# Kernel optimization log

Hardware: AMD Instinct MI355X
Metric: run time of the kernel (lower is better)

## Reference

```python
import jax, jax.numpy as jnp
import numpy as np

D_MODEL = 512
D_STATE = 16
D_INNER = 2 * D_MODEL  # expand_factor=2
IN_CH = 256
B_SZ, H_SZ, W_SZ = 4, 32, 32


def setup_inputs() -> dict:
    key = jax.random.key(0)
    ks = jax.random.split(key, 24)
    f = jax.random.normal
    inp = {}
    inp["x_V"] = f(ks[0], (B_SZ, IN_CH, H_SZ, W_SZ), jnp.float32)
    inp["x_I"] = f(ks[1], (B_SZ, IN_CH, H_SZ, W_SZ), jnp.float32)
    # channel_reduce: 1x1 conv + BN (inference stats)
    inp["conv_red_w"] = f(ks[2], (D_MODEL, IN_CH), jnp.float32) * 0.05
    inp["bn_red_g"] = jnp.ones((D_MODEL,), jnp.float32)
    inp["bn_red_b"] = jnp.zeros((D_MODEL,), jnp.float32)
    inp["bn_red_m"] = jnp.zeros((D_MODEL,), jnp.float32)
    inp["bn_red_v"] = jnp.ones((D_MODEL,), jnp.float32)
    # channel_restore: 1x1 conv + BN
    inp["conv_res_w"] = f(ks[3], (IN_CH, D_MODEL), jnp.float32) * 0.05
    inp["bn_res_g"] = jnp.ones((IN_CH,), jnp.float32)
    inp["bn_res_b"] = jnp.zeros((IN_CH,), jnp.float32)
    inp["bn_res_m"] = jnp.zeros((IN_CH,), jnp.float32)
    inp["bn_res_v"] = jnp.ones((IN_CH,), jnp.float32)
    # lambda_predictor convs (1x1 on pooled features == linear)
    inp["lam_w1"] = f(ks[4], (D_MODEL // 4, D_MODEL * 2), jnp.float32) * 0.05
    inp["lam_b1"] = jnp.zeros((D_MODEL // 4,), jnp.float32)
    inp["lam_w2"] = f(ks[5], (2, D_MODEL // 4), jnp.float32) * 0.05
    inp["lam_b2"] = jnp.zeros((2,), jnp.float32)
    # two SimplifiedMamba2Blocks
    for i, p in enumerate(["V", "I"]):
        kk = jax.random.split(ks[6 + i], 6)
        inp[p + "_in_w"] = f(kk[0], (2 * D_INNER, D_MODEL), jnp.float32) * 0.03
        inp[p + "_out_w"] = f(kk[1], (D_MODEL, D_INNER), jnp.float32) * 0.03
        # A = -exp(A_log) in (-1, -0.05): stable decay
        inp[p + "_A_log"] = jnp.log(jax.random.uniform(kk[2], (D_INNER, D_STATE), jnp.float32, 0.05, 0.95))
        inp[p + "_B"] = f(kk[3], (D_INNER, D_STATE), jnp.float32) * 0.05
        inp[p + "_C"] = jnp.full((D_INNER, D_STATE), 0.01, jnp.float32)
        inp[p + "_ln_g"] = jnp.ones((D_MODEL,), jnp.float32)
        inp[p + "_ln_b"] = jnp.zeros((D_MODEL,), jnp.float32)
    inp["gate"] = jnp.asarray(0.1, jnp.float32)
    return inp


def _bn(x, g, b, m, v):
    # x: (B,C,H,W); inference-mode batchnorm
    return (x - m[:, None, None]) / jnp.sqrt(v[:, None, None] + 1e-5) * g[:, None, None] + b[:, None, None]


def _conv1x1(x, w):
    return jnp.einsum('bchw,oc->bohw', x, w)


def _ssm_scan(x_ssm, A, Bm, Cm, reverse):
    # x_ssm: (B,L,I); A,Bm,Cm: (I,S)
    bsz = x_ssm.shape[0]
    h0 = jnp.zeros((bsz, A.shape[0], A.shape[1]), x_ssm.dtype)

    def step(h, xt):  # xt: (B,I)
        h = jnp.clip(h * A + xt[:, :, None] * Bm, -10.0, 10.0)
        return h, jnp.einsum('bis,is->bi', h, Cm)

    _, ys = jax.lax.scan(step, h0, jnp.swapaxes(x_ssm, 0, 1), reverse=reverse)
    return jnp.swapaxes(ys, 0, 1)  # (B,L,I), in original time order


def _mamba(x, ln_g, ln_b, in_w, out_w, A_log, Bm, Cm):
    # LayerNorm
    mu = jnp.mean(x, -1, keepdims=True)
    var = jnp.mean((x - mu) ** 2, -1, keepdims=True)
    xn = (x - mu) / jnp.sqrt(var + 1e-5) * ln_g + ln_b
    xp = xn @ in_w.T  # (B,L,2*I)
    x_ssm, gate = jnp.split(xp, 2, axis=-1)
    A = jnp.clip(-jnp.exp(A_log), -10.0, -0.01)
    yf = _ssm_scan(x_ssm, A, Bm, Cm, False)
    yb = _ssm_scan(x_ssm, A, Bm, Cm, True)
    out = 0.5 * (yf + yb) * jax.nn.silu(gate)
    return out @ out_w.T


def reference(x_V, x_I, conv_red_w, bn_red_g, bn_red_b, bn_red_m, bn_red_v,
              conv_res_w, bn_res_g, bn_res_b, bn_res_m, bn_res_v,
              lam_w1, lam_b1, lam_w2, lam_b2,
              V_in_w, V_out_w, V_A_log, V_B, V_C, V_ln_g, V_ln_b,
              I_in_w, I_out_w, I_A_log, I_B, I_C, I_ln_g, I_ln_b, gate):
    B, _, H, W = x_V.shape
    xVr = jax.nn.relu(_bn(_conv1x1(x_V, conv_red_w), bn_red_g, bn_red_b, bn_red_m, bn_red_v))
    xIr = jax.nn.relu(_bn(_conv1x1(x_I, conv_red_w), bn_red_g, bn_red_b, bn_red_m, bn_red_v))
    # same spatial size -> adaptive pooling and [:B] slicing are identities
    conc = jnp.concatenate([xVr, xIr], axis=1)  # (B, 2*d_model, H, W)

    def lam(c):
        p = jnp.mean(c, axis=(2, 3))  # global avg pool -> (B, 2*d_model)
        h1 = jax.nn.relu(p @ lam_w1.T + lam_b1)
        return jax.nn.softmax(h1 @ lam_w2.T + lam_b2, axis=-1)  # (B,2)

    lamV = lam(conc)
    lamI = lam(conc)

    seq_V = jnp.swapaxes(xVr.reshape(B, D_MODEL, H * W), 1, 2)  # (B,L,D)
    seq_I = jnp.swapaxes(xIr.reshape(B, D_MODEL, H * W), 1, 2)

    outV_std = _mamba(seq_V, V_ln_g, V_ln_b, V_in_w, V_out_w, V_A_log, V_B, V_C)
    outI_std = _mamba(seq_I, I_ln_g, I_ln_b, I_in_w, I_out_w, I_A_log, I_B, I_C)
    outV_cross = _mamba(seq_V, V_ln_g, V_ln_b, V_in_w, V_out_w, V_A_log, jax.lax.stop_gradient(I_B), V_C)
    outI_cross = _mamba(seq_I, I_ln_g, I_ln_b, I_in_w, I_out_w, I_A_log, jax.lax.stop_gradient(V_B), I_C)

    outV = lamV[:, 0][:, None, None] * outV_std + lamV[:, 1][:, None, None] * outV_cross
    outI = lamI[:, 0][:, None, None] * outI_std + lamI[:, 1][:, None, None] * outI_cross

    featV = jnp.swapaxes(outV, 1, 2).reshape(B, D_MODEL, H, W)
    featI = jnp.swapaxes(outI, 1, 2).reshape(B, D_MODEL, H, W)
    featV = _bn(_conv1x1(featV, conv_res_w), bn_res_g, bn_res_b, bn_res_m, bn_res_v)
    featI = _bn(_conv1x1(featI, conv_res_w), bn_res_g, bn_res_b, bn_res_m, bn_res_v)

    g = jax.nn.sigmoid(gate)
    return (x_V + g * featV, x_I + g * featI)
```

## Files before the change

kernel.cpp:

```cpp
#include <hip/hip_runtime.h>
#include <hip/hip_bf16.h>
#include <math.h>

#define L_SZ 1024
#define DM   512
#define DI   1024
#define NS   16
#define CH   256

typedef float4 f4;
typedef __attribute__((ext_vector_type(8))) short short8;
typedef __attribute__((ext_vector_type(8))) unsigned short u16x8;
typedef __attribute__((ext_vector_type(4))) float f32x4;

__device__ __forceinline__ float bf2f(ushort u) {
    union { unsigned int i; float f; } x; x.i = ((unsigned int)u) << 16; return x.f;
}
__device__ __forceinline__ ushort f2bf(float f) {
    union { float f; unsigned int i; } x; x.f = f;
    unsigned int r = x.i + 0x7FFFu + ((x.i >> 16) & 1u);
    return (ushort)(r >> 16);
}
__device__ __forceinline__ uint pkbf(float a, float b) {
    union { __hip_bfloat162 h; uint u; } c;
    c.h = __float22bfloat162_rn(make_float2(a, b));
    return c.u;
}

#define GLOAD16(gp, lp) \
  __builtin_amdgcn_global_load_lds((const __attribute__((address_space(1))) void*)(gp), \
                                   (__attribute__((address_space(3))) void*)(lp), 16, 0, 0)

__global__ __launch_bounds__(256) void k_prep(
    const float* __restrict__ s0, const float* __restrict__ s1,
    const float* __restrict__ s2, const float* __restrict__ s3,
    const float* __restrict__ s4, const float* __restrict__ s5,
    ushort* __restrict__ d0, ushort* __restrict__ d1,
    ushort* __restrict__ d2, ushort* __restrict__ d3,
    ushort* __restrict__ d4, ushort* __restrict__ d5,
    const float* __restrict__ xv, const float* __restrict__ xi,
    ushort* __restrict__ xtv, ushort* __restrict__ xti,
    float* __restrict__ p, unsigned int* __restrict__ cnt)
{
    __shared__ float tile[32][36];
    const int bid = blockIdx.x;
    const int t = threadIdx.x;
    if (bid < 2304) {
        const float* s; ushort* d; int rel;
        if      (bid < 128)  { s = s0; d = d0; rel = bid; }
        else if (bid < 256)  { s = s1; d = d1; rel = bid - 128; }
        else if (bid < 1280) { s = s2; d = d2; rel = bid - 256; }
        else                 { s = s3; d = d3; rel = bid - 1280; }
        const int i = rel * 256 + t;
        f4 v = ((const f4*)s)[i];
        ushort4 o;
        o.x = f2bf(v.x); o.y = f2bf(v.y); o.z = f2bf(v.z); o.w = f2bf(v.w);
        ((ushort4*)d)[i] = o;
        return;
    }
    if (bid < 3328) {
        const int rel = (bid < 2816) ? bid - 2304 : bid - 2816;
        const float* wo = (bid < 2816) ? s4 : s5;
        ushort* wt      = (bid < 2816) ? d4 : d5;
        const int kt = rel & 31, dt = rel >> 5;
        const int d0_ = dt * 32, k0 = kt * 32;
        {
            int cc = t >> 3, ll4 = (t & 7) << 2;
            f4 v = *(const f4*)(wo + (size_t)(d0_ + cc) * 1024 + k0 + ll4);
            tile[cc][ll4 + 0] = v.x; tile[cc][ll4 + 1] = v.y;
            tile[cc][ll4 + 2] = v.z; tile[cc][ll4 + 3] = v.w;
        }
        __syncthreads();
        {
            int ll = t >> 3, cc4 = (t & 7) << 2;
            ushort4 o;
            o.x = f2bf(tile[cc4 + 0][ll]); o.y = f2bf(tile[cc4 + 1][ll]);
            o.z = f2bf(tile[cc4 + 2][ll]); o.w = f2bf(tile[cc4 + 3][ll]);
            *(ushort4*)(wt + (size_t)(k0 + ll) * 512 + d0_ + cc4) = o;
        }
        return;
    }
    if (bid < 5376) {
        const int rel = bid - 3328;
        const int l0 = (rel & 31) * 32, c0 = ((rel >> 5) & 7) * 32;
        const int z = rel >> 8;
        const int b = z & 3, st = z >> 2;
        const float* x = st ? xi : xv;
        ushort* xt = st ? xti : xtv;
        {
            int cc = t >> 3, ll4 = (t & 7) << 2;
            f4 v = *(const f4*)(x + ((size_t)(b * CH + c0 + cc)) * L_SZ + l0 + ll4);
            tile[cc][ll4 + 0] = v.x; tile[cc][ll4 + 1] = v.y;
            tile[cc][ll4 + 2] = v.z; tile[cc][ll4 + 3] = v.w;
        }
        __syncthreads();
        {
            int ll = t >> 3, cc4 = (t & 7) << 2;
            ushort4 o;
            o.x = f2bf(tile[cc4 + 0][ll]); o.y = f2bf(tile[cc4 + 1][ll]);
            o.z = f2bf(tile[cc4 + 2][ll]); o.w = f2bf(tile[cc4 + 3][ll]);
            *(ushort4*)(xt + ((size_t)(b * L_SZ + l0 + ll)) * CH + c0 + cc4) = o;
        }
        return;
    }
    const f4 z4 = {0.f, 0.f, 0.f, 0.f};
    ((f4*)p)[t]       = z4;
    ((f4*)p)[t + 256] = z4;
    ((f4*)p)[t + 512] = z4;
    ((f4*)p)[t + 768] = z4;
    if (t == 0) *cnt = 0u;
}

template<int MODE, int BM, int BN, int OS>
__global__ __launch_bounds__(256) void k_gemm(
    const ushort* __restrict__ A0, const ushort* __restrict__ A1,
    const ushort* __restrict__ B0, const ushort* __restrict__ B1,
    int K,
    float* __restrict__ o0, float* __restrict__ o1,
    ushort* __restrict__ ob0, ushort* __restrict__ ob1,
    ushort* __restrict__ sb0, ushort* __restrict__ sb1,
    const float* __restrict__ pg, const float* __restrict__ pb,
    const float* __restrict__ pm, const float* __restrict__ pv,
    const float* __restrict__ x0, const float* __restrict__ x1,
    const float* __restrict__ gate, float* __restrict__ pp)
{
    constexpr int MT   = BM / 32;
    constexpr int NT   = BN / 32;
    constexpr int ASEG = BM / 16;
    constexpr int NSEG = (BM + BN) / 16;
    constexpr int SPW  = NSEG / 4;
    __shared__ __align__(16) ushort Sl[2][(BM + BN) * 32];
    const int t = threadIdx.x;
    const int wv = t >> 6, lane = t & 63;
    const int n0 = blockIdx.x * BN, m0 = blockIdx.y * BM;
    const int st = blockIdx.z;
    const ushort* Ap = st ? A1 : A0;
    const ushort* Bp = st ? B1 : B0;
    const int wm = wv >> 1, wn = wv & 1;
    const int lrow = lane & 15, q = lane >> 4;
    f32x4 acc[MT][NT];
    #pragma unroll
    for (int a_ = 0; a_ < MT; ++a_)
        #pragma unroll
        for (int b_ = 0; b_ < NT; ++b_)
            acc[a_][b_] = (f32x4){0.f, 0.f, 0.f, 0.f};
    const int srow = lane >> 2;
    const int skk  = (((lane & 3) ^ ((lane >> 3) & 3)) << 3);
    const int koff = ((q ^ ((lrow >> 1) & 3)) << 3);
    #pragma unroll
    for (int s2 = 0; s2 < SPW; ++s2) {
        const int seg = wv * SPW + s2;
        const int grow = (seg < ASEG) ? (m0 + seg * 16 + srow)
                                      : (n0 + (seg - ASEG) * 16 + srow);
        const ushort* src = (seg < ASEG) ? Ap : Bp;
        GLOAD16(src + (size_t)grow * K + skk, &Sl[0][seg * 512]);
    }
    int cur = 0;
    for (int k0 = 0; k0 < K; k0 += 32) {
        if (k0 + 32 < K) {
            #pragma unroll
            for (int s2 = 0; s2 < SPW; ++s2) {
                const int seg = wv * SPW + s2;
                const int grow = (seg < ASEG) ? (m0 + seg * 16 + srow)
                                              : (n0 + (seg - ASEG) * 16 + srow);
                const ushort* src = (seg < ASEG) ? Ap : Bp;
                GLOAD16(src + (size_t)grow * K + (k0 + 32) + skk, &Sl[cur ^ 1][seg * 512]);
            }
            if constexpr (SPW == 2)      asm volatile("s_waitcnt vmcnt(2)" ::: "memory");
            else if constexpr (SPW == 3) asm volatile("s_waitcnt vmcnt(3)" ::: "memory");
            else                         asm volatile("s_waitcnt vmcnt(4)" ::: "memory");
        } else {
            asm volatile("s_waitcnt vmcnt(0)" ::: "memory");
        }
        __builtin_amdgcn_s_barrier();
        short8 af[MT], bfr[NT];
        #pragma unroll
        for (int mt = 0; mt < MT; ++mt)
            af[mt] = *(const short8*)&Sl[cur][(wm * (MT * 16) + mt * 16 + lrow) * 32 + koff];
        #pragma unroll
        for (int nt = 0; nt < NT; ++nt)
            bfr[nt] = *(const short8*)&Sl[cur][(BM + wn * (NT * 16) + nt * 16 + lrow) * 32 + koff];
        #pragma unroll
        for (int mt = 0; mt < MT; ++mt)
            #pragma unroll
            for (int nt = 0; nt < NT; ++nt) {
                if constexpr (MODE == 1)
                    acc[mt][nt] = __builtin_amdgcn_mfma_f32_16x16x32_bf16(bfr[nt], af[mt], acc[mt][nt], 0, 0, 0);
                else
                    acc[mt][nt] = __builtin_amdgcn_mfma_f32_16x16x32_bf16(af[mt], bfr[nt], acc[mt][nt], 0, 0, 0);
            }
        asm volatile("s_waitcnt lgkmcnt(0)" ::: "memory");
        __builtin_amdgcn_sched_barrier(0);
        __builtin_amdgcn_s_barrier();
        cur ^= 1;
    }
    if (MODE == 0) {
        ushort* sq = st ? ob1 : ob0;
        const int b = m0 >> 10;
        #pragma unroll
        for (int nt = 0; nt < NT; ++nt) {
            const int gn = n0 + wn * (NT * 16) + nt * 16 + lrow;
            const float s  = pg[gn] * rsqrtf(pv[gn] + 1e-5f);
            const float sh = pb[gn] - pm[gn] * s;
            float psum = 0.f;
            #pragma unroll
            for (int mt = 0; mt < MT; ++mt) {
                const int gm = m0 + wm * (MT * 16) + mt * 16 + q * 4;
                float v[4];
                #pragma unroll
                for (int r = 0; r < 4; ++r) {
                    v[r] = fmaxf(fmaf(acc[mt][nt][r], s, sh), 0.f);
                    psum += v[r];
                }
                const uint u01 = pkbf(v[0], v[1]);
                const uint u23 = pkbf(v[2], v[3]);
                ushort* bp = sq + (size_t)gm * DM + gn;
                bp[0]      = (ushort)u01;
                bp[DM]     = (ushort)(u01 >> 16);
                bp[2 * DM] = (ushort)u23;
                bp[3 * DM] = (ushort)(u23 >> 16);
            }
            psum += __shfl_xor(psum, 16, 64);
            psum += __shfl_xor(psum, 32, 64);
            if (q == 0)
                atomicAdd(pp + (b * 1024 + st * 512 + gn), psum * (1.0f / 1024.0f));
        }
    } else if (MODE == 1) {
        const bool isx = (n0 < 1024);
        ushort* xp = st ? ob1 : ob0;
        ushort* sp = st ? sb1 : sb0;
        #pragma unroll
        for (int mt = 0; mt < MT; ++mt) {
            const int gm = m0 + wm * (MT * 16) + mt * 16 + lrow;
            #pragma unroll
            for (int nt = 0; nt < NT; ++nt) {
                const int gnb = n0 + wn * (NT * 16) + nt * 16 + q * 4;
                if (isx) {
                    const uint u01 = pkbf(acc[mt][nt][0], acc[mt][nt][1]);
                    const uint u23 = pkbf(acc[mt][nt][2], acc[mt][nt][3]);
                    *(uint2*)(xp + (size_t)gm * DI + gnb) = make_uint2(u01, u23);
                } else {
                    float sv[4];
                    #pragma unroll
                    for (int r = 0; r < 4; ++r) {
                        const float v = acc[mt][nt][r];
                        sv[r] = v / (1.f + __expf(-v));
                    }
                    const uint u01 = pkbf(sv[0], sv[1]);
                    const uint u23 = pkbf(sv[2], sv[3]);
                    *(uint2*)(sp + (size_t)gm * DI + gnb - 1024) = make_uint2(u01, u23);
                }
            }
        }
    } else if (MODE == 2) {
        ushort* fp_ = st ? ob1 : ob0;
        #pragma unroll
        for (int nt = 0; nt < NT; ++nt) {
            const int gn = n0 + wn * (NT * 16) + nt * 16 + lrow;
            #pragma unroll
            for (int mt = 0; mt < MT; ++mt) {
                const int gm = m0 + wm * (MT * 16) + mt * 16 + q * 4;
                const uint u01 = pkbf(acc[mt][nt][0], acc[mt][nt][1]);
                const uint u23 = pkbf(acc[mt][nt][2], acc[mt][nt][3]);
                ushort* bp = fp_ + (size_t)gm * OS + gn;
                bp[0]      = (ushort)u01;
                bp[OS]     = (ushort)(u01 >> 16);
                bp[2 * OS] = (ushort)u23;
                bp[3 * OS] = (ushort)(u23 >> 16);
            }
        }
    } else {
        const float* xin = st ? x1 : x0;
        float* op = st ? o1 : o0;
        const float g = 1.f / (1.f + __expf(-gate[0]));
        #pragma unroll
        for (int nt = 0; nt < NT; ++nt) {
            const int gn = n0 + wn * (NT * 16) + nt * 16 + lrow;
            const float s  = pg[gn] * rsqrtf(pv[gn] + 1e-5f);
            const float sh = pb[gn] - pm[gn] * s;
            #pragma unroll
            for (int mt = 0; mt < MT; ++mt) {
                const int gmb = m0 + wm * (MT * 16) + mt * 16 + q * 4;
                const int b = gmb >> 10, l = gmb & 1023;
                const size_t off = ((size_t)(b * CH + gn)) * L_SZ + l;
                f4 xi = *(const f4*)(xin + off);
                f4 o;
                o.x = xi.x + g * fmaf(acc[mt][nt][0], s, sh);
                o.y = xi.y + g * fmaf(acc[mt][nt][1], s, sh);
                o.z = xi.z + g * fmaf(acc[mt][nt][2], s, sh);
                o.w = xi.w + g * fmaf(acc[mt][nt][3], s, sh);
                *(f4*)(op + off) = o;
            }
        }
    }
}

__global__ __launch_bounds__(256) void k_lam(
    const float* __restrict__ p, const float* __restrict__ w1,
    const float* __restrict__ b1, const float* __restrict__ w2,
    const float* __restrict__ b2, float* __restrict__ h1,
    float* __restrict__ lam, unsigned int* __restrict__ cnt)
{
    __shared__ float lsm[8];
    __shared__ unsigned int tick;
    const int t = threadIdx.x, lane = t & 63, wv = t >> 6;
    const int idx = blockIdx.x * 4 + wv;
    const int b = idx >> 7, j = idx & 127;
    const float* pb = p + b * 1024;
    const float* wr = w1 + j * 1024;
    float s = 0.f;
    #pragma unroll
    for (int k = 0; k < 16; ++k)
        s = fmaf(pb[lane + k * 64], wr[lane + k * 64], s);
    #pragma unroll
    for (int off = 1; off < 64; off <<= 1) s += __shfl_xor(s, off, 64);
    if (lane == 0) h1[idx] = fmaxf(s + b1[j], 0.f);
    __threadfence();
    __syncthreads();
    if (t == 0) tick = atomicAdd(cnt, 1u);
    __syncthreads();
    if (tick != 127u) return;
    __threadfence();
    {
        const int g32 = t >> 5, l32 = t & 31;
        const int bb = g32 >> 1, kk = g32 & 1;
        const float* hb = h1 + bb * 128;
        const float* wr2 = w2 + kk * 128;
        float ss = 0.f;
        #pragma unroll
        for (int u = 0; u < 4; ++u)
            ss = fmaf(hb[l32 + u * 32], wr2[l32 + u * 32], ss);
        #pragma unroll
        for (int off = 1; off < 32; off <<= 1) ss += __shfl_xor(ss, off, 64);
        if (l32 == 0) lsm[g32] = ss + b2[kk];
    }
    __syncthreads();
    if (t < 4) {
        const float a0 = lsm[t * 2], a1 = lsm[t * 2 + 1];
        const float m  = fmaxf(a0, a1);
        const float e0 = __expf(a0 - m), e1 = __expf(a1 - m);
        const float inv = 1.f / (e0 + e1);
        lam[t * 2 + 0] = e0 * inv;
        lam[t * 2 + 1] = e1 * inv;
    }
}

__global__ __launch_bounds__(256) void k_ln(
    const ushort* __restrict__ seq0, const ushort* __restrict__ seq1,
    const float* __restrict__ g0, const float* __restrict__ b0,
    const float* __restrict__ g1, const float* __restrict__ b1,
    ushort* __restrict__ ln0, ushort* __restrict__ ln1)
{
    const int t = threadIdx.x, lane = t & 63, wv = t >> 6;
    const int row = blockIdx.x * 4 + wv, st = blockIdx.y;
    const ushort* seq = st ? seq1 : seq0;
    const float* gg  = st ? g1 : g0;
    const float* bb  = st ? b1 : b0;
    ushort* ln = st ? ln1 : ln0;
    const u16x8 v = *(const u16x8*)(seq + (size_t)row * DM + lane * 8);
    float f[8];
    float s = 0.f, ss = 0.f;
    #pragma unroll
    for (int i = 0; i < 8; ++i) {
        f[i] = bf2f(v[i]);
        s += f[i];
        ss = fmaf(f[i], f[i], ss);
    }
    #pragma unroll
    for (int off = 1; off < 64; off <<= 1) {
        s += __shfl_xor(s, off, 64); ss += __shfl_xor(ss, off, 64);
    }
    const float mu = s * (1.f / 512.f);
    const float rstd = rsqrtf(ss * (1.f / 512.f) - mu * mu + 1e-5f);
    const f4 gv0 = *(const f4*)(gg + lane * 8);
    const f4 gv1 = *(const f4*)(gg + lane * 8 + 4);
    const f4 bv0 = *(const f4*)(bb + lane * 8);
    const f4 bv1 = *(const f4*)(bb + lane * 8 + 4);
    const float gvv[8] = {gv0.x, gv0.y, gv0.z, gv0.w, gv1.x, gv1.y, gv1.z, gv1.w};
    const float bvv[8] = {bv0.x, bv0.y, bv0.z, bv0.w, bv1.x, bv1.y, bv1.z, bv1.w};
    u16x8 o;
    #pragma unroll
    for (int i = 0; i < 8; i += 2) {
        const uint u = pkbf(fmaf((f[i]     - mu) * rstd, gvv[i],     bvv[i]),
                            fmaf((f[i + 1] - mu) * rstd, gvv[i + 1], bvv[i + 1]));
        o[i]     = (ushort)u;
        o[i + 1] = (ushort)(u >> 16);
    }
    *(u16x8*)(ln + (size_t)row * DM + lane * 8) = o;
}

__global__ __launch_bounds__(128, 4) void k_scan(
    const ushort* __restrict__ xsV, const ushort* __restrict__ xsI,
    const ushort* __restrict__ sgV, const ushort* __restrict__ sgI,
    const float* __restrict__ VA, const float* __restrict__ VB,
    const float* __restrict__ VC, const float* __restrict__ IA,
    const float* __restrict__ IB, const float* __restrict__ IC,
    const float* __restrict__ lam,
    ushort* __restrict__ yV, ushort* __restrict__ yI)
{
    __shared__ __align__(16) ushort xf[3][16][64];
    __shared__ __align__(16) ushort xb[3][16][64];
    const int t = threadIdx.x;
    const int shalf = t & 1;
    const int il = t >> 1;
    const int b = blockIdx.y;
    const int st = blockIdx.z >> 4, j = blockIdx.z & 15;
    const int c0 = blockIdx.x * 64;
    const ushort* xrow  = (st ? xsI : xsV) + (size_t)b * L_SZ * DI + c0;
    const ushort* sgrow = (st ? sgI : sgV) + (size_t)b * L_SZ * DI + c0;
    ushort* yrow        = (st ? yI  : yV ) + (size_t)b * L_SZ * DI + c0;
    const float* Alog = st ? IA : VA;
    const float* Cm   = st ? IC : VC;
    const float* Bown = st ? IB : VB;
    const float* Both = st ? VB : IB;
    const float lam0 = lam[b * 2 + 0], lam1 = lam[b * 2 + 1];
    float a[8], w[8], gf[8], gb[8];
    const int base = (c0 + il) * NS + shalf * 8;
    #pragma unroll
    for (int s = 0; s < 8; ++s) {
        a[s] = fminf(fmaxf(-__expf(Alog[base + s]), -10.f), -0.01f);
        w[s] = 0.5f * Cm[base + s] * fmaf(lam0, Bown[base + s], lam1 * Both[base + s]);
        gf[s] = 0.f; gb[s] = 0.f;
    }
    const int row0 = j << 6;
    const int srow = t >> 3;
    const int scol = (t & 7) << 3;
    ushort stash[32];

#define STAGE(PH, BUF) do { \
    int rf_ = row0 - 64 + (PH) * 16 + srow; rf_ = max(0, min(1023, rf_)); \
    GLOAD16(xrow + (size_t)rf_ * DI + scol, &xf[BUF][srow][0]); \
    int rb_ = row0 + 127 - (PH) * 16 - srow; rb_ = max(0, min(1023, rb_)); \
    GLOAD16(xrow + (size_t)rb_ * DI + scol, &xb[BUF][srow][0]); \
} while (0)

#define WBODY(BUF) \
    _Pragma("unroll") \
    for (int n = 0; n < 16; ++n) { \
        const float vf = bf2f(xf[BUF][n][il]); \
        const float vb = bf2f(xb[BUF][n][il]); \
        _Pragma("unroll") \
        for (int s = 0; s < 8; ++s) { \
            gf[s] = fmaf(a[s], gf[s], vf); \
            gb[s] = fmaf(a[s], gb[s], vb); \
        } \
    }

#define SBODY(MB, BUF) \
    _Pragma("unroll") \
    for (int n = 0; n < 16; ++n) { \
        const float vf = bf2f(xf[BUF][n][il]); \
        const float vb = bf2f(xb[BUF][n][il]); \
        float yf = 0.f, yb = 0.f; \
        _Pragma("unroll") \
        for (int s = 0; s < 8; ++s) { \
            gf[s] = fmaf(a[s], gf[s], vf); yf = fmaf(gf[s], w[s], yf); \
            gb[s] = fmaf(a[s], gb[s], vb); yb = fmaf(gb[s], w[s], yb); \
        } \
        yf += __shfl_xor(yf, 1, 64); \
        yb += __shfl_xor(yb, 1, 64); \
        stash[(MB) + n] = f2bf(shalf ? yf : yb); \
    }

#define FBODY(MB, BUF) \
    _Pragma("unroll") \
    for (int n = 0; n < 16; ++n) { \
        const float vf = bf2f(xf[BUF][n][il]); \
        const float vb = bf2f(xb[BUF][n][il]); \
        float yf = 0.f, yb = 0.f; \
        _Pragma("unroll") \
        for (int s = 0; s < 8; ++s) { \
            gf[s] = fmaf(a[s], gf[s], vf); yf = fmaf(gf[s], w[s], yf); \
            gb[s] = fmaf(a[s], gb[s], vb); yb = fmaf(gb[s], w[s], yb); \
        } \
        yf += __shfl_xor(yf, 1, 64); \
        yb += __shfl_xor(yb, 1, 64); \
        const int m_ = (MB) + n; \
        const int r_ = row0 + (shalf ? (63 - m_) : m_); \
        const float own_ = shalf ? yb : yf; \
        const float z_ = (own_ + bf2f(stash[63 - m_])) \
                       * bf2f(sgrow[(size_t)r_ * DI + il]); \
        yrow[(size_t)r_ * DI + il] = f2bf(z_); \
    }

#define VMW(N) asm volatile("s_waitcnt vmcnt(" #N ")" ::: "memory")

    STAGE(0, 0);
    STAGE(1, 1); VMW(2); __builtin_amdgcn_s_barrier(); WBODY(0);
    STAGE(2, 2); VMW(2); __builtin_amdgcn_s_barrier(); WBODY(1);
    STAGE(3, 0); VMW(2); __builtin_amdgcn_s_barrier(); WBODY(2);
    STAGE(4, 1); VMW(2); __builtin_amdgcn_s_barrier(); WBODY(0);
    STAGE(5, 2); VMW(2); __builtin_amdgcn_s_barrier();
    if (j == 0) {
        #pragma unroll
        for (int s = 0; s < 8; ++s) gf[s] = 0.f;
    }
    if (j == 15) {
        #pragma unroll
        for (int s = 0; s < 8; ++s) gb[s] = 0.f;
    }
    SBODY(0, 1);
    STAGE(6, 0); VMW(2); __builtin_amdgcn_s_barrier(); SBODY(16, 2);
    STAGE(7, 1); VMW(2); __builtin_amdgcn_s_barrier(); FBODY(32, 0);
    VMW(32);             __builtin_amdgcn_s_barrier(); FBODY(48, 1);

#undef STAGE
#undef WBODY
#undef SBODY
#undef FBODY
#undef VMW
}

extern "C" void kernel_launch(void* const* d_in, const int* in_sizes, int n_in,
                              void* d_out, int out_size, void* d_ws, size_t ws_size,
                              hipStream_t stream)
{
    const float* xV       = (const float*)d_in[0];
    const float* xI       = (const float*)d_in[1];
    const float* convredw = (const float*)d_in[2];
    const float* bnredg   = (const float*)d_in[3];
    const float* bnredb   = (const float*)d_in[4];
    const float* bnredm   = (const float*)d_in[5];
    const float* bnredv   = (const float*)d_in[6];
    const float* convresw = (const float*)d_in[7];
    const float* bnresg   = (const float*)d_in[8];
    const float* bnresb   = (const float*)d_in[9];
    const float* bnresm   = (const float*)d_in[10];
    const float* bnresv   = (const float*)d_in[11];
    const float* lamw1    = (const float*)d_in[12];
    const float* lamb1    = (const float*)d_in[13];
    const float* lamw2    = (const float*)d_in[14];
    const float* lamb2    = (const float*)d_in[15];
    const float* Vinw     = (const float*)d_in[16];
    const float* Voutw    = (const float*)d_in[17];
    const float* VAlog    = (const float*)d_in[18];
    const float* VB       = (const float*)d_in[19];
    const float* VC       = (const float*)d_in[20];
    const float* Vlng     = (const float*)d_in[21];
    const float* Vlnb     = (const float*)d_in[22];
    const float* Iinw     = (const float*)d_in[23];
    const float* Ioutw    = (const float*)d_in[24];
    const float* IAlog    = (const float*)d_in[25];
    const float* IB       = (const float*)d_in[26];
    const float* IC       = (const float*)d_in[27];
    const float* Ilng     = (const float*)d_in[28];
    const float* Ilnb     = (const float*)d_in[29];
    const float* gate     = (const float*)d_in[30];

    char* W = (char*)d_ws;
    const size_t MB = 1048576;
    ushort* seqV  = (ushort*)(W + 0);
    ushort* seqI  = (ushort*)(W + 4  * MB);
    float*  p     = (float*)(W + 8 * MB);
    float*  lam   = (float*)(W + 8 * MB + 16384);
    float*  h1    = (float*)(W + 8 * MB + 32768);
    unsigned int* cnt = (unsigned int*)(W + 8 * MB + 49152);
    ushort* sgV   = (ushort*)(W + 17 * MB);
    ushort* sgI   = (ushort*)(W + 25 * MB);
    ushort* yV    = (ushort*)(W + 33 * MB);
    ushort* yI    = (ushort*)(W + 41 * MB);
    ushort* wred  = (ushort*)(W + 65 * MB);
    ushort* wres  = (ushort*)(W + 65 * MB + 262144);
    ushort* winV  = (ushort*)(W + 66 * MB);
    ushort* winI  = (ushort*)(W + 68 * MB);
    ushort* woTv  = (ushort*)(W + 70 * MB);
    ushort* woTi  = (ushort*)(W + 71 * MB);
    ushort* xtV   = (ushort*)(W + 72 * MB);
    ushort* xtI   = (ushort*)(W + 74 * MB);
    ushort* lnV   = (ushort*)(W + 76 * MB);
    ushort* lnI   = (ushort*)(W + 80 * MB);
    ushort* xsV   = (ushort*)(W + 84 * MB);
    ushort* xsI   = (ushort*)(W + 92 * MB);
    ushort* wcombV = (ushort*)(W + 100 * MB);
    ushort* wcombI = (ushort*)(W + 100 * MB + 524288);
    float*  outp  = (float*)d_out;

    k_prep<<<dim3(5377), 256, 0, stream>>>(
        convredw, convresw, Vinw, Iinw, Voutw, Ioutw,
        wred, wres, winV, winI, woTv, woTi,
        xV, xI, xtV, xtI, p, cnt);
    k_gemm<2, 64, 64, 1024><<<dim3(16, 4, 2), 256, 0, stream>>>(
        wres, wres, woTv, woTi, 512,
        nullptr, nullptr, wcombV, wcombI, nullptr, nullptr,
        nullptr, nullptr, nullptr, nullptr, nullptr, nullptr, nullptr, nullptr);
    k_gemm<0, 128, 64, 512><<<dim3(8, 32, 2), 256, 0, stream>>>(xtV, xtI, wred, wred, 256,
        nullptr, nullptr, seqV, seqI, nullptr, nullptr,
        bnredg, bnredb, bnredm, bnredv, nullptr, nullptr, nullptr, p);
    k_lam<<<128, 256, 0, stream>>>(p, lamw1, lamb1, lamw2, lamb2, h1, lam, cnt);
    k_ln<<<dim3(1024, 2), 256, 0, stream>>>(seqV, seqI, Vlng, Vlnb, Ilng, Ilnb, lnV, lnI);
    k_gemm<1, 128, 128, 512><<<dim3(16, 32, 2), 256, 0, stream>>>(lnV, lnI, winV, winI, 512,
        nullptr, nullptr, xsV, xsI, sgV, sgI,
        nullptr, nullptr, nullptr, nullptr, nullptr, nullptr, nullptr, nullptr);
    k_scan<<<dim3(16, 4, 32), 128, 0, stream>>>(xsV, xsI, sgV, sgI,
        VAlog, VB, VC, IAlog, IB, IC, lam, yV, yI);
    k_gemm<3, 64, 64, 512><<<dim3(4, 64, 2), 256, 0, stream>>>(yV, yI, wcombV, wcombI, 1024,
        outp, outp + 1048576, nullptr, nullptr, nullptr, nullptr,
        bnresg, bnresb, bnresm, bnresv, xV, xI, gate, nullptr);
}
```

Baseline: 243.8 us.

## Restructure bidirectional scan: one thread per direction over 128-row chunks

The scan kernel now gives each thread one direction and all 16 states, instead of splitting the states across a thread pair that runs both directions. Each block loads a 256-row window into shared memory in one go instead of a triple-buffered staged pipeline. The chunk grows from 64 to 128 rows, so the grid halves and the warm-up recompute per output row drops. The forward and backward halves are combined through a shuffle of packed bf16 pairs. This trades per-block parallelism and occupancy (launch bounds lowered to 2, 32 KB of LDS) for less redundant warm-up work and fewer reductions.

```diff
diff --git a/kernel.cpp b/kernel.cpp
--- a/kernel.cpp
+++ b/kernel.cpp
@@ -389,7 +389,7 @@
     *(u16x8*)(ln + (size_t)row * DM + lane * 8) = o;
 }
 
-__global__ __launch_bounds__(128, 4) void k_scan(
+__global__ __launch_bounds__(128, 2) void k_scan(
     const ushort* __restrict__ xsV, const ushort* __restrict__ xsI,
     const ushort* __restrict__ sgV, const ushort* __restrict__ sgI,
     const float* __restrict__ VA, const float* __restrict__ VB,
@@ -398,13 +398,12 @@
     const float* __restrict__ lam,
     ushort* __restrict__ yV, ushort* __restrict__ yI)
 {
-    __shared__ __align__(16) ushort xf[3][16][64];
-    __shared__ __align__(16) ushort xb[3][16][64];
+    __shared__ __align__(16) ushort xt[256][64];
     const int t = threadIdx.x;
-    const int shalf = t & 1;
+    const int dir = t & 1;
     const int il = t >> 1;
     const int b = blockIdx.y;
-    const int st = blockIdx.z >> 4, j = blockIdx.z & 15;
+    const int st = blockIdx.z >> 3, j = blockIdx.z & 7;
     const int c0 = blockIdx.x * 64;
     const ushort* xrow  = (st ? xsI : xsV) + (size_t)b * L_SZ * DI + c0;
     const ushort* sgrow = (st ? sgI : sgV) + (size_t)b * L_SZ * DI + c0;
@@ -414,101 +413,107 @@
     const float* Bown = st ? IB : VB;
     const float* Both = st ? VB : IB;
     const float lam0 = lam[b * 2 + 0], lam1 = lam[b * 2 + 1];
-    float a[8], w[8], gf[8], gb[8];
-    const int base = (c0 + il) * NS + shalf * 8;
-    #pragma unroll
-    for (int s = 0; s < 8; ++s) {
-        a[s] = fminf(fmaxf(-__expf(Alog[base + s]), -10.f), -0.01f);
-        w[s] = 0.5f * Cm[base + s] * fmaf(lam0, Bown[base + s], lam1 * Both[base + s]);
-        gf[s] = 0.f; gb[s] = 0.f;
-    }
-    const int row0 = j << 6;
+    const int row0 = j << 7;
     const int srow = t >> 3;
     const int scol = (t & 7) << 3;
-    ushort stash[32];
-
-#define STAGE(PH, BUF) do { \
-    int rf_ = row0 - 64 + (PH) * 16 + srow; rf_ = max(0, min(1023, rf_)); \
-    GLOAD16(xrow + (size_t)rf_ * DI + scol, &xf[BUF][srow][0]); \
-    int rb_ = row0 + 127 - (PH) * 16 - srow; rb_ = max(0, min(1023, rb_)); \
-    GLOAD16(xrow + (size_t)rb_ * DI + scol, &xb[BUF][srow][0]); \
-} while (0)
-
-#define WBODY(BUF) \
+    #pragma unroll
+    for (int i = 0; i < 16; ++i) {
+        int r = row0 - 64 + i * 16 + srow;
+        r = max(0, min(1023, r));
+        GLOAD16(xrow + (size_t)r * DI + scol, &xt[i * 16 + srow][0]);
+    }
+    float a[16], w[16], g[16];
+    {
+        const int cb = (c0 + il) * NS;
+        #pragma unroll
+        for (int s4 = 0; s4 < 4; ++s4) {
+            const f4 av = *(const f4*)(Alog + cb + s4 * 4);
+            const f4 cv = *(const f4*)(Cm   + cb + s4 * 4);
+            const f4 bo = *(const f4*)(Bown + cb + s4 * 4);
+            const f4 bt = *(const f4*)(Both + cb + s4 * 4);
+            const float avv[4] = {av.x, av.y, av.z, av.w};
+            const float cvv[4] = {cv.x, cv.y, cv.z, cv.w};
+            const float bov[4] = {bo.x, bo.y, bo.z, bo.w};
+            const float btv[4] = {bt.x, bt.y, bt.z, bt.w};
+            #pragma unroll
+            for (int q = 0; q < 4; ++q) {
+                const int s = s4 * 4 + q;
+                a[s] = fminf(fmaxf(-__expf(avv[q]), -10.f), -0.01f);
+                w[s] = 0.5f * cvv[q] * fmaf(lam0, bov[q], lam1 * btv[q]);
+                g[s] = 0.f;
+            }
+        }
+    }
+    __syncthreads();
+
+    const ushort* xtf = &xt[0][0];
+    int toff = (dir ? 255 : 0) * 64 + il;
+    const int tstep = dir ? -64 : 64;
+
+    #pragma unroll
+    for (int n = 0; n < 64; ++n) {
+        const float v = bf2f(xtf[toff]); toff += tstep;
+        #pragma unroll
+        for (int s = 0; s < 16; ++s) g[s] = fmaf(a[s], g[s], v);
+    }
+    if ((j == 0 && dir == 0) || (j == 7 && dir == 1)) {
+        #pragma unroll
+        for (int s = 0; s < 16; ++s) g[s] = 0.f;
+    }
+
+#define SROW(Y) { \
+    const float v_ = bf2f(xtf[toff]); toff += tstep; \
+    float ye_ = 0.f, yo_ = 0.f; \
     _Pragma("unroll") \
-    for (int n = 0; n < 16; ++n) { \
-        const float vf = bf2f(xf[BUF][n][il]); \
-        const float vb = bf2f(xb[BUF][n][il]); \
-        _Pragma("unroll") \
-        for (int s = 0; s < 8; ++s) { \
-            gf[s] = fmaf(a[s], gf[s], vf); \
-            gb[s] = fmaf(a[s], gb[s], vb); \
-        } \
-    }
-
-#define SBODY(MB, BUF) \
-    _Pragma("unroll") \
-    for (int n = 0; n < 16; ++n) { \
-        const float vf = bf2f(xf[BUF][n][il]); \
-        const float vb = bf2f(xb[BUF][n][il]); \
-        float yf = 0.f, yb = 0.f; \
-        _Pragma("unroll") \
-        for (int s = 0; s < 8; ++s) { \
-            gf[s] = fmaf(a[s], gf[s], vf); yf = fmaf(gf[s], w[s], yf); \
-            gb[s] = fmaf(a[s], gb[s], vb); yb = fmaf(gb[s], w[s], yb); \
-        } \
-        yf += __shfl_xor(yf, 1, 64); \
-        yb += __shfl_xor(yb, 1, 64); \
-        stash[(MB) + n] = f2bf(shalf ? yf : yb); \
-    }
-
-#define FBODY(MB, BUF) \
-    _Pragma("unroll") \
-    for (int n = 0; n < 16; ++n) { \
-        const float vf = bf2f(xf[BUF][n][il]); \
-        const float vb = bf2f(xb[BUF][n][il]); \
-        float yf = 0.f, yb = 0.f; \
-        _Pragma("unroll") \
-        for (int s = 0; s < 8; ++s) { \
-            gf[s] = fmaf(a[s], gf[s], vf); yf = fmaf(gf[s], w[s], yf); \
-            gb[s] = fmaf(a[s], gb[s], vb); yb = fmaf(gb[s], w[s], yb); \
-        } \
-        yf += __shfl_xor(yf, 1, 64); \
-        yb += __shfl_xor(yb, 1, 64); \
-        const int m_ = (MB) + n; \
-        const int r_ = row0 + (shalf ? (63 - m_) : m_); \
-        const float own_ = shalf ? yb : yf; \
-        const float z_ = (own_ + bf2f(stash[63 - m_])) \
-                       * bf2f(sgrow[(size_t)r_ * DI + il]); \
-        yrow[(size_t)r_ * DI + il] = f2bf(z_); \
-    }
-
-#define VMW(N) asm volatile("s_waitcnt vmcnt(" #N ")" ::: "memory")
-
-    STAGE(0, 0);
-    STAGE(1, 1); VMW(2); __builtin_amdgcn_s_barrier(); WBODY(0);
-    STAGE(2, 2); VMW(2); __builtin_amdgcn_s_barrier(); WBODY(1);
-    STAGE(3, 0); VMW(2); __builtin_amdgcn_s_barrier(); WBODY(2);
-    STAGE(4, 1); VMW(2); __builtin_amdgcn_s_barrier(); WBODY(0);
-    STAGE(5, 2); VMW(2); __builtin_amdgcn_s_barrier();
-    if (j == 0) {
-        #pragma unroll
-        for (int s = 0; s < 8; ++s) gf[s] = 0.f;
-    }
-    if (j == 15) {
-        #pragma unroll
-        for (int s = 0; s < 8; ++s) gb[s] = 0.f;
-    }
-    SBODY(0, 1);
-    STAGE(6, 0); VMW(2); __builtin_amdgcn_s_barrier(); SBODY(16, 2);
-    STAGE(7, 1); VMW(2); __builtin_amdgcn_s_barrier(); FBODY(32, 0);
-    VMW(32);             __builtin_amdgcn_s_barrier(); FBODY(48, 1);
-
-#undef STAGE
-#undef WBODY
-#undef SBODY
-#undef FBODY
-#undef VMW
+    for (int s = 0; s < 8; ++s) { \
+        g[s]     = fmaf(a[s],     g[s],     v_); ye_ = fmaf(g[s],     w[s],     ye_); \
+        g[s + 8] = fmaf(a[s + 8], g[s + 8], v_); yo_ = fmaf(g[s + 8], w[s + 8], yo_); \
+    } \
+    Y = ye_ + yo_; }
+
+#define SPAIR(WREG) { \
+    float y0_, y1_; SROW(y0_) SROW(y1_) \
+    WREG = (uint)f2bf(y0_) | ((uint)f2bf(y1_) << 16); }
+
+#define FPAIR(K, WREG) { \
+    const uint p_ = __shfl_xor(WREG, 1, 64); \
+    float y0_, y1_; \
+    SROW(y0_) \
+    { const int r_ = row0 + (dir ? (63 - 2 * (K)) : (64 + 2 * (K))); \
+      const float z_ = (y0_ + bf2f((ushort)(p_ >> 16))) \
+                     * bf2f(sgrow[(size_t)r_ * DI + il]); \
+      yrow[(size_t)r_ * DI + il] = f2bf(z_); } \
+    SROW(y1_) \
+    { const int r_ = row0 + (dir ? (62 - 2 * (K)) : (65 + 2 * (K))); \
+      const float z_ = (y1_ + bf2f((ushort)(p_ & 0xFFFFu))) \
+                     * bf2f(sgrow[(size_t)r_ * DI + il]); \
+      yrow[(size_t)r_ * DI + il] = f2bf(z_); } }
+
+    uint s00, s01, s02, s03, s04, s05, s06, s07;
+    uint s08, s09, s10, s11, s12, s13, s14, s15;
+    uint s16, s17, s18, s19, s20, s21, s22, s23;
+    uint s24, s25, s26, s27, s28, s29, s30, s31;
+
+    SPAIR(s00) SPAIR(s01) SPAIR(s02) SPAIR(s03)
+    SPAIR(s04) SPAIR(s05) SPAIR(s06) SPAIR(s07)
+    SPAIR(s08) SPAIR(s09) SPAIR(s10) SPAIR(s11)
+    SPAIR(s12) SPAIR(s13) SPAIR(s14) SPAIR(s15)
+    SPAIR(s16) SPAIR(s17) SPAIR(s18) SPAIR(s19)
+    SPAIR(s20) SPAIR(s21) SPAIR(s22) SPAIR(s23)
+    SPAIR(s24) SPAIR(s25) SPAIR(s26) SPAIR(s27)
+    SPAIR(s28) SPAIR(s29) SPAIR(s30) SPAIR(s31)
+    FPAIR(0,  s31) FPAIR(1,  s30) FPAIR(2,  s29) FPAIR(3,  s28)
+    FPAIR(4,  s27) FPAIR(5,  s26) FPAIR(6,  s25) FPAIR(7,  s24)
+    FPAIR(8,  s23) FPAIR(9,  s22) FPAIR(10, s21) FPAIR(11, s20)
+    FPAIR(12, s19) FPAIR(13, s18) FPAIR(14, s17) FPAIR(15, s16)
+    FPAIR(16, s15) FPAIR(17, s14) FPAIR(18, s13) FPAIR(19, s12)
+    FPAIR(20, s11) FPAIR(21, s10) FPAIR(22, s09) FPAIR(23, s08)
+    FPAIR(24, s07) FPAIR(25, s06) FPAIR(26, s05) FPAIR(27, s04)
+    FPAIR(28, s03) FPAIR(29, s02) FPAIR(30, s01) FPAIR(31, s00)
+
+#undef SROW
+#undef SPAIR
+#undef FPAIR
 }
 
 extern "C" void kernel_launch(void* const* d_in, const int* in_sizes, int n_in,
@@ -591,7 +596,7 @@
     k_gemm<1, 128, 128, 512><<<dim3(16, 32, 2), 256, 0, stream>>>(lnV, lnI, winV, winI, 512,
         nullptr, nullptr, xsV, xsI, sgV, sgI,
         nullptr, nullptr, nullptr, nullptr, nullptr, nullptr, nullptr, nullptr);
-    k_scan<<<dim3(16, 4, 32), 128, 0, stream>>>(xsV, xsI, sgV, sgI,
+    k_scan<<<dim3(16, 4, 16), 128, 0, stream>>>(xsV, xsI, sgV, sgI,
         VAlog, VB, VC, IAlog, IB, IC, lam, yV, yI);
     k_gemm<3, 64, 64, 512><<<dim3(4, 64, 2), 256, 0, stream>>>(yV, yI, wcombV, wcombI, 1024,
         outp, outp + 1048576, nullptr, nullptr, nullptr, nullptr,
```

Result: faster. 232.4 us (-4.7%).
